# Kernel tuning notes

Hardware: AMD Instinct MI355X
Metric: run time of the kernel (lower is better)

The kernel has to match this reference:

```python
import jax, jax.numpy as jnp
import numpy as np
import math

BLUR, P, SCALING = 0.05, 2.0, 0.9
DIAMETER = 8.0  # static bound on max |x-y| for unit-normal 1-D data (geomloss derives it from data)
NEG = -1e9     # masked log-weight


def _eps_schedule():
    # geomloss epsilon_schedule: diameter^p -> blur^p, geometric with ratio scaling^p
    eps = [DIAMETER ** P]
    eps += list(np.exp(np.arange(P * math.log(DIAMETER), P * math.log(BLUR), P * math.log(SCALING))))
    eps += [BLUR ** P]
    return np.asarray(eps, dtype=np.float32)


def _softmin(eps, C, h):
    # h: [m] = log-weights + dual/eps ; returns [n] = -eps*logsumexp_j(h_j - C_ij/eps)
    return -eps * jax.nn.logsumexp(h[None, :] - C / eps, axis=1)


def _sinkhorn_divergence(x, y, logw):
    # x, y: [B] 1-D point clouds for one output dim; logw: [B] masked log-weights.
    # Debiased Sinkhorn divergence S = OT_eps(a,b) - 0.5 OT(a,a) - 0.5 OT(b,b), p=2 cost |x-y|^2/2.
    Cxy = 0.5 * (x[:, None] - y[None, :]) ** 2
    Cxx = 0.5 * (x[:, None] - x[None, :]) ** 2
    Cyy = 0.5 * (y[:, None] - y[None, :]) ** 2
    eps_list = jnp.asarray(_eps_schedule())
    e0 = eps_list[0]
    f = _softmin(e0, Cxy, logw)    # dual on x for OT(a,b)
    g = _softmin(e0, Cxy.T, logw)  # dual on y for OT(a,b)
    a = _softmin(e0, Cxx, logw)    # self dual on x
    b = _softmin(e0, Cyy, logw)    # self dual on y

    def step(carry, eps):
        f, g, a, b = carry
        ft = _softmin(eps, Cxy, logw + g / eps)
        gt = _softmin(eps, Cxy.T, logw + f / eps)
        at = _softmin(eps, Cxx, logw + a / eps)
        bt = _softmin(eps, Cyy, logw + b / eps)
        return (0.5 * (f + ft), 0.5 * (g + gt), 0.5 * (a + at), 0.5 * (b + bt)), None

    (f, g, a, b), _ = jax.lax.scan(step, (f, g, a, b), eps_list)
    # last extrapolation at final eps (full updates, no damping)
    e = eps_list[-1]
    f, g = _softmin(e, Cxy, logw + g / e), _softmin(e, Cxy.T, logw + f / e)
    a = 0.5 * (a + _softmin(e, Cxx, logw + a / e))
    b = 0.5 * (b + _softmin(e, Cyy, logw + b / e))
    w = jnp.exp(logw)  # 1/n on valid samples, 0 on masked
    return jnp.sum(w * (f - a)) + jnp.sum(w * (g - b))


def reference(predictions, targets):
    # predictions, targets: [B, D]; NaNs in targets mark invalid samples per dim
    mask = ~jnp.isnan(targets)                      # [B, D]
    y = jnp.where(mask, targets, 0.0)
    counts = jnp.sum(mask, axis=0)                  # [D]
    logn = jnp.log(jnp.maximum(counts, 1).astype(predictions.dtype))
    logw = jnp.where(mask, -logn[None, :], NEG)     # [B, D]
    per_dim = jax.vmap(_sinkhorn_divergence, in_axes=(1, 1, 1))(predictions, y, logw)
    per_dim = jnp.where(counts > 1, per_dim, 0.0)   # dims with <=1 valid sample -> 0
    total = jnp.mean(per_dim)                       # weights=None -> mean over dims
    return total, per_dim


def setup_inputs() -> dict:
    key = jax.random.key(0)
    k1, k2, k3 = jax.random.split(key, 3)
    B, D = 2048, 8
    preds = jax.random.normal(k1, (B, D), dtype=jnp.float32)
    targ = jax.random.normal(k2, (B, D), dtype=jnp.float32)
    nan_mask = jax.random.uniform(k3, (B, D)) < 0.1
    targ = jnp.where(nan_mask, jnp.nan, targ)
    return {"predictions": preds, "targets": targ}
```

## Files before the change

kernel.cpp:

```cpp
#include <hip/hip_runtime.h>
#include <math.h>

#define BN 2048
#define DN 8
#define NEGW -1e9f
#define TPB 256
#define RPB 64
#define JSPLIT 8
#define SLOTS (BN/2)
#define SPC (SLOTS/JSPLIT)

static __device__ __forceinline__ float wave_reduce_sum(float v){
  #pragma unroll
  for (int off = 32; off > 0; off >>= 1) v += __shfl_xor(v, off, 64);
  return v;
}

__global__ void setup_kernel(const float* __restrict__ pred, const float* __restrict__ targ,
                             float* __restrict__ xcol, float* __restrict__ ycol,
                             float* __restrict__ logw, float* __restrict__ counts){
  int d = blockIdx.x;
  int t = threadIdx.x;
  int lane = t & 63, wave = t >> 6;
  float mk[BN/256];
  float c = 0.f;
  for (int k = 0; k < BN/256; k++){
    int i = t + k*256;
    float tv = targ[i*DN + d];
    bool m = !(tv != tv);
    mk[k] = m ? 1.f : 0.f;
    c += mk[k];
    ycol[d*BN + i] = m ? tv : 0.f;
    xcol[d*BN + i] = pred[i*DN + d];
  }
  __shared__ float sh[4];
  __shared__ float logn_sh;
  float cw = wave_reduce_sum(c);
  if (lane == 0) sh[wave] = cw;
  __syncthreads();
  if (t == 0){
    float tot = sh[0] + sh[1] + sh[2] + sh[3];
    counts[d] = tot;
    logn_sh = logf(fmaxf(tot, 1.f));
  }
  __syncthreads();
  float ln = logn_sh;
  for (int k = 0; k < BN/256; k++){
    int i = t + k*256;
    logw[d*BN + i] = (mk[k] > 0.f) ? -ln : NEGW;
  }
}

__global__ __launch_bounds__(TPB) void sink_step(
      const float* __restrict__ xcol, const float* __restrict__ ycol,
      const float* __restrict__ logw,
      const float* __restrict__ dold, float* __restrict__ dnew,
      float eps, float inv_eps, int mode){
  const float L2E = 1.44269504088896340736f;
  const float LN2 = 0.69314718055994530942f;
  __shared__ float4 pair4[SLOTS];
  __shared__ float pm[JSPLIT][RPB];
  __shared__ float ps[JSPLIT][RPB];

  int bid = blockIdx.x;
  int rc  = bid & 31;
  int mat = (bid >> 5) & 3;
  int d   = bid >> 7;
  int t   = threadIdx.x;
  int rs  = t & 31;
  int jc  = t >> 5;

  const float* xb = xcol + d*BN;
  const float* yb = ycol + d*BN;
  const float* lw = logw + d*BN;
  const float* ri; const float* pj; int hsel;
  switch (mat){
    case 0:  ri = xb; pj = yb; hsel = 1; break;
    case 1:  ri = yb; pj = xb; hsel = 0; break;
    case 2:  ri = xb; pj = xb; hsel = 2; break;
    default: ri = yb; pj = yb; hsel = 3; break;
  }
  const float* hd  = dold + (size_t)hsel*DN*BN + d*BN;
  const float* dmp = dold + (size_t)mat *DN*BN + d*BN;
  float*       op  = dnew + (size_t)mat *DN*BN + d*BN;

  const float c1 = L2E * inv_eps;
  const float c2 = 0.5f * inv_eps * L2E;

  const float2* pj2 = (const float2*)pj;
  const float2* lw2 = (const float2*)lw;
  const float2* hd2 = (const float2*)hd;
  #pragma unroll
  for (int k = 0; k < BN/2/TPB; k++){
    int idx = t + k*TPB;
    float2 y2 = pj2[idx];
    float2 l2 = lw2[idx];
    float h0 = l2.x, h1 = l2.y;
    if (mode != 0){
      float2 dd = hd2[idx];
      h0 = fmaf(dd.x, inv_eps, h0);
      h1 = fmaf(dd.y, inv_eps, h1);
    }
    pair4[idx] = make_float4(y2.x, fmaf(-c2*y2.x, y2.x, L2E*h0),
                             y2.y, fmaf(-c2*y2.y, y2.y, L2E*h1));
  }

  int row0 = rc*RPB + rs;
  int row1 = row0 + 32;
  float xi0 = ri[row0], xi1 = ri[row1];
  float alpha0 = c1 * xi0, beta0 = c2 * xi0 * xi0;
  float alpha1 = c1 * xi1, beta1 = c2 * xi1 * xi1;
  __syncthreads();

  int q0 = jc * SPC;
  float m00=-INFINITY, m01=-INFINITY, m10=-INFINITY, m11=-INFINITY;
  #pragma unroll 4
  for (int q = 0; q < SPC; q += 2){
    float4 A = pair4[q0+q];
    float4 B = pair4[q0+q+1];
    m00 = fmaxf(m00, fmaf(alpha0, A.x, A.y));
    m01 = fmaxf(m01, fmaf(alpha0, A.z, A.w));
    m10 = fmaxf(m10, fmaf(alpha1, A.x, A.y));
    m11 = fmaxf(m11, fmaf(alpha1, A.z, A.w));
    m00 = fmaxf(m00, fmaf(alpha0, B.x, B.y));
    m01 = fmaxf(m01, fmaf(alpha0, B.z, B.w));
    m10 = fmaxf(m10, fmaf(alpha1, B.x, B.y));
    m11 = fmaxf(m11, fmaf(alpha1, B.z, B.w));
  }
  pm[jc][rs]      = fmaxf(m00, m01);
  pm[jc][rs+32]   = fmaxf(m10, m11);
  __syncthreads();
  float m0 = -INFINITY, m1 = -INFINITY;
  #pragma unroll
  for (int k = 0; k < JSPLIT; k++){
    m0 = fmaxf(m0, pm[k][rs]);
    m1 = fmaxf(m1, pm[k][rs+32]);
  }

  float s00=0.f, s01=0.f, s10=0.f, s11=0.f;
  #pragma unroll 4
  for (int q = 0; q < SPC; q += 2){
    float4 A = pair4[q0+q];
    float4 B = pair4[q0+q+1];
    s00 += __builtin_amdgcn_exp2f(fmaf(alpha0, A.x, A.y) - m0);
    s01 += __builtin_amdgcn_exp2f(fmaf(alpha0, A.z, A.w) - m0);
    s10 += __builtin_amdgcn_exp2f(fmaf(alpha1, A.x, A.y) - m1);
    s11 += __builtin_amdgcn_exp2f(fmaf(alpha1, A.z, A.w) - m1);
    s00 += __builtin_amdgcn_exp2f(fmaf(alpha0, B.x, B.y) - m0);
    s01 += __builtin_amdgcn_exp2f(fmaf(alpha0, B.z, B.w) - m0);
    s10 += __builtin_amdgcn_exp2f(fmaf(alpha1, B.x, B.y) - m1);
    s11 += __builtin_amdgcn_exp2f(fmaf(alpha1, B.z, B.w) - m1);
  }
  ps[jc][rs]    = (s00+s01);
  ps[jc][rs+32] = (s10+s11);
  __syncthreads();

  if (t < RPB){
    int row = rc*RPB + t;
    float s = 0.f;
    float m = -INFINITY;
    #pragma unroll
    for (int k = 0; k < JSPLIT; k++){
      s += ps[k][t];
      m  = fmaxf(m, pm[k][t]);
    }
    float beta = (t < 32) ? beta0 : beta1;
    float lse2 = (m + __builtin_amdgcn_logf(s)) - beta;
    float tn = -eps * (LN2 * lse2);
    float outv;
    if (mode == 1 || (mode == 2 && mat >= 2)) outv = 0.5f * (dmp[row] + tn);
    else                                      outv = tn;
    op[row] = outv;
  }
}

__global__ void reduce_kernel(const float* __restrict__ dual, const float* __restrict__ logw,
                              const float* __restrict__ counts, float* __restrict__ out){
  int d = blockIdx.x;
  int t = threadIdx.x;
  int lane = t & 63, wave = t >> 6;
  float acc = 0.f;
  for (int k = 0; k < BN/256; k++){
    int i = t + k*256;
    float w  = expf(logw[d*BN + i]);
    float fv = dual[0*DN*BN + d*BN + i];
    float gv = dual[1*DN*BN + d*BN + i];
    float av = dual[2*DN*BN + d*BN + i];
    float bv = dual[3*DN*BN + d*BN + i];
    acc += w * ((fv - av) + (gv - bv));
  }
  __shared__ float sh[4];
  float aw = wave_reduce_sum(acc);
  if (lane == 0) sh[wave] = aw;
  __syncthreads();
  if (t == 0){
    float tot = sh[0] + sh[1] + sh[2] + sh[3];
    out[1 + d] = (counts[d] > 1.5f) ? tot : 0.f;
  }
}

__global__ void total_kernel(float* __restrict__ out){
  if (threadIdx.x == 0 && blockIdx.x == 0){
    float s = 0.f;
    for (int d = 0; d < DN; d++) s += out[1 + d];
    out[0] = s / (float)DN;
  }
}

extern "C" void kernel_launch(void* const* d_in, const int* in_sizes, int n_in,
                              void* d_out, int out_size, void* d_ws, size_t ws_size,
                              hipStream_t stream){
  const float* pred = (const float*)d_in[0];
  const float* targ = (const float*)d_in[1];
  float* out = (float*)d_out;
  float* ws  = (float*)d_ws;

  float* xcol   = ws;
  float* ycol   = ws + (size_t)DN*BN;
  float* logw   = ws + (size_t)2*DN*BN;
  float* counts = ws + (size_t)3*DN*BN;
  float* buf0   = ws + (size_t)3*DN*BN + 64;
  float* buf1   = buf0 + (size_t)4*DN*BN;

  float eps_list[64]; int n = 0;
  {
    const double P = 2.0, DIAM = 8.0, BLUR = 0.05, SC = 0.9;
    double ls = P*log(DIAM), le = P*log(BLUR), st = P*log(SC);
    eps_list[n++] = (float)pow(DIAM, P);
    int cnt = (int)ceil((le - ls)/st);
    for (int k = 0; k < cnt; k++) eps_list[n++] = (float)exp(ls + st*(double)k);
    eps_list[n++] = (float)(BLUR*BLUR);
  }

  setup_kernel<<<DN, 256, 0, stream>>>(pred, targ, xcol, ycol, logw, counts);

  dim3 grid(DN*4*32), blk(TPB);
  float* cur = buf0; float* nxt = buf1;
  {
    float e = eps_list[0];
    sink_step<<<grid, blk, 0, stream>>>(xcol, ycol, logw, cur, cur, e, 1.f/e, 0);
  }
  for (int k = 0; k < n; k++){
    float e = eps_list[k];
    sink_step<<<grid, blk, 0, stream>>>(xcol, ycol, logw, cur, nxt, e, 1.f/e, 1);
    float* tmp = cur; cur = nxt; nxt = tmp;
  }
  {
    float e = eps_list[n-1];
    sink_step<<<grid, blk, 0, stream>>>(xcol, ycol, logw, cur, nxt, e, 1.f/e, 2);
    float* tmp = cur; cur = nxt; nxt = tmp;
  }
  reduce_kernel<<<DN, 256, 0, stream>>>(cur, logw, counts, out);
  total_kernel<<<1, 64, 0, stream>>>(out);
}
```

Baseline: 1.205 ms.

## Process four rows per thread with packed float2 FMA/max in sinkhorn step

Doubles rows per block from 64 to 128, so each thread now handles four rows and the grid halves. Each shared-memory pair load is reused across more rows, and the FMA and max math uses two-wide vector types so the compiler can emit packed FP32 instructions. The row maximum is reduced once into shared memory instead of by every thread. The trade-off is fewer blocks (512), which may underfill the GPU, plus higher register pressure. The exp2 work per element is unchanged.

```diff
diff --git a/kernel.cpp b/kernel.cpp
--- a/kernel.cpp
+++ b/kernel.cpp
@@ -5,10 +5,13 @@
 #define DN 8
 #define NEGW -1e9f
 #define TPB 256
-#define RPB 64
+#define RPB 128
+#define RS 32
 #define JSPLIT 8
 #define SLOTS (BN/2)
 #define SPC (SLOTS/JSPLIT)
+
+typedef float f2 __attribute__((ext_vector_type(2)));
 
 static __device__ __forceinline__ float wave_reduce_sum(float v){
   #pragma unroll
@@ -61,13 +64,14 @@
   __shared__ float4 pair4[SLOTS];
   __shared__ float pm[JSPLIT][RPB];
   __shared__ float ps[JSPLIT][RPB];
+  __shared__ float mmx[RPB];
 
   int bid = blockIdx.x;
-  int rc  = bid & 31;
-  int mat = (bid >> 5) & 3;
-  int d   = bid >> 7;
+  int rc  = bid & 15;
+  int mat = (bid >> 4) & 3;
+  int d   = bid >> 6;
   int t   = threadIdx.x;
-  int rs  = t & 31;
+  int rs  = t & (RS-1);
   int jc  = t >> 5;
 
   const float* xb = xcol + d*BN;
@@ -91,7 +95,7 @@
   const float2* lw2 = (const float2*)lw;
   const float2* hd2 = (const float2*)hd;
   #pragma unroll
-  for (int k = 0; k < BN/2/TPB; k++){
+  for (int k = 0; k < SLOTS/TPB; k++){
     int idx = t + k*TPB;
     float2 y2 = pj2[idx];
     float2 l2 = lw2[idx];
@@ -101,70 +105,85 @@
       h0 = fmaf(dd.x, inv_eps, h0);
       h1 = fmaf(dd.y, inv_eps, h1);
     }
-    pair4[idx] = make_float4(y2.x, fmaf(-c2*y2.x, y2.x, L2E*h0),
-                             y2.y, fmaf(-c2*y2.y, y2.y, L2E*h1));
+    pair4[idx] = make_float4(y2.x, y2.y,
+                             fmaf(-c2*y2.x, y2.x, L2E*h0),
+                             fmaf(-c2*y2.y, y2.y, L2E*h1));
   }
 
   int row0 = rc*RPB + rs;
-  int row1 = row0 + 32;
-  float xi0 = ri[row0], xi1 = ri[row1];
-  float alpha0 = c1 * xi0, beta0 = c2 * xi0 * xi0;
-  float alpha1 = c1 * xi1, beta1 = c2 * xi1 * xi1;
+  f2 a2[4];
+  #pragma unroll
+  for (int r = 0; r < 4; r++){
+    float xi = ri[row0 + 32*r];
+    float al = c1 * xi;
+    a2[r] = (f2){al, al};
+  }
   __syncthreads();
 
   int q0 = jc * SPC;
-  float m00=-INFINITY, m01=-INFINITY, m10=-INFINITY, m11=-INFINITY;
-  #pragma unroll 4
+  f2 m2[4];
+  #pragma unroll
+  for (int r = 0; r < 4; r++) m2[r] = (f2){-INFINITY, -INFINITY};
+  #pragma unroll 2
   for (int q = 0; q < SPC; q += 2){
     float4 A = pair4[q0+q];
     float4 B = pair4[q0+q+1];
-    m00 = fmaxf(m00, fmaf(alpha0, A.x, A.y));
-    m01 = fmaxf(m01, fmaf(alpha0, A.z, A.w));
-    m10 = fmaxf(m10, fmaf(alpha1, A.x, A.y));
-    m11 = fmaxf(m11, fmaf(alpha1, A.z, A.w));
-    m00 = fmaxf(m00, fmaf(alpha0, B.x, B.y));
-    m01 = fmaxf(m01, fmaf(alpha0, B.z, B.w));
-    m10 = fmaxf(m10, fmaf(alpha1, B.x, B.y));
-    m11 = fmaxf(m11, fmaf(alpha1, B.z, B.w));
-  }
-  pm[jc][rs]      = fmaxf(m00, m01);
-  pm[jc][rs+32]   = fmaxf(m10, m11);
-  __syncthreads();
-  float m0 = -INFINITY, m1 = -INFINITY;
-  #pragma unroll
-  for (int k = 0; k < JSPLIT; k++){
-    m0 = fmaxf(m0, pm[k][rs]);
-    m1 = fmaxf(m1, pm[k][rs+32]);
-  }
-
-  float s00=0.f, s01=0.f, s10=0.f, s11=0.f;
-  #pragma unroll 4
+    f2 yA = (f2){A.x, A.y}, hA = (f2){A.z, A.w};
+    f2 yB = (f2){B.x, B.y}, hB = (f2){B.z, B.w};
+    #pragma unroll
+    for (int r = 0; r < 4; r++){
+      m2[r] = __builtin_elementwise_max(m2[r], __builtin_elementwise_fma(a2[r], yA, hA));
+      m2[r] = __builtin_elementwise_max(m2[r], __builtin_elementwise_fma(a2[r], yB, hB));
+    }
+  }
+  #pragma unroll
+  for (int r = 0; r < 4; r++) pm[jc][rs + 32*r] = fmaxf(m2[r].x, m2[r].y);
+  __syncthreads();
+
+  if (t < RPB){
+    float m = -INFINITY;
+    #pragma unroll
+    for (int k = 0; k < JSPLIT; k++) m = fmaxf(m, pm[k][t]);
+    mmx[t] = m;
+  }
+  __syncthreads();
+
+  f2 mb[4];
+  #pragma unroll
+  for (int r = 0; r < 4; r++){
+    float m = mmx[rs + 32*r];
+    mb[r] = (f2){m, m};
+  }
+
+  f2 s2[4];
+  #pragma unroll
+  for (int r = 0; r < 4; r++) s2[r] = (f2){0.f, 0.f};
+  #pragma unroll 2
   for (int q = 0; q < SPC; q += 2){
     float4 A = pair4[q0+q];
     float4 B = pair4[q0+q+1];
-    s00 += __builtin_amdgcn_exp2f(fmaf(alpha0, A.x, A.y) - m0);
-    s01 += __builtin_amdgcn_exp2f(fmaf(alpha0, A.z, A.w) - m0);
-    s10 += __builtin_amdgcn_exp2f(fmaf(alpha1, A.x, A.y) - m1);
-    s11 += __builtin_amdgcn_exp2f(fmaf(alpha1, A.z, A.w) - m1);
-    s00 += __builtin_amdgcn_exp2f(fmaf(alpha0, B.x, B.y) - m0);
-    s01 += __builtin_amdgcn_exp2f(fmaf(alpha0, B.z, B.w) - m0);
-    s10 += __builtin_amdgcn_exp2f(fmaf(alpha1, B.x, B.y) - m1);
-    s11 += __builtin_amdgcn_exp2f(fmaf(alpha1, B.z, B.w) - m1);
-  }
-  ps[jc][rs]    = (s00+s01);
-  ps[jc][rs+32] = (s10+s11);
+    f2 yA = (f2){A.x, A.y}, hA = (f2){A.z, A.w};
+    f2 yB = (f2){B.x, B.y}, hB = (f2){B.z, B.w};
+    #pragma unroll
+    for (int r = 0; r < 4; r++){
+      f2 vA = __builtin_elementwise_fma(a2[r], yA, hA) - mb[r];
+      f2 vB = __builtin_elementwise_fma(a2[r], yB, hB) - mb[r];
+      s2[r] += (f2){__builtin_amdgcn_exp2f(vA.x), __builtin_amdgcn_exp2f(vA.y)};
+      s2[r] += (f2){__builtin_amdgcn_exp2f(vB.x), __builtin_amdgcn_exp2f(vB.y)};
+    }
+  }
+  #pragma unroll
+  for (int r = 0; r < 4; r++) ps[jc][rs + 32*r] = s2[r].x + s2[r].y;
   __syncthreads();
 
   if (t < RPB){
     int row = rc*RPB + t;
     float s = 0.f;
-    float m = -INFINITY;
-    #pragma unroll
-    for (int k = 0; k < JSPLIT; k++){
-      s += ps[k][t];
-      m  = fmaxf(m, pm[k][t]);
-    }
-    float beta = (t < 32) ? beta0 : beta1;
+    #pragma unroll
+    for (int k = 0; k < JSPLIT; k++) s += ps[k][t];
+    float m  = mmx[t];
+    float xi = ri[row];
+    float beta = c2 * xi * xi;
     float lse2 = (m + __builtin_amdgcn_logf(s)) - beta;
     float tn = -eps * (LN2 * lse2);
     float outv;
@@ -234,7 +253,7 @@
 
   setup_kernel<<<DN, 256, 0, stream>>>(pred, targ, xcol, ycol, logw, counts);
 
-  dim3 grid(DN*4*32), blk(TPB);
+  dim3 grid(DN*4*16), blk(TPB);
   float* cur = buf0; float* nxt = buf1;
   {
     float e = eps_list[0];
```

Result: no change. 1.197 ms (-0.7%).
